# Performance work log

Measured on AMD Instinct MI355X. Metric: run time of the kernel, lower is better.

The kernel has to match this reference:

```python
import jax, jax.numpy as jnp
import numpy as np

D_MODEL = 1024
NUM_HEADS = 16
D_K = D_MODEL // NUM_HEADS
NEG_INF = -1000000000.0  # matches masked_fill value in the torch source


def setup_inputs() -> dict:
    key = jax.random.key(0)
    ks = jax.random.split(key, 12)
    B, S, D = 2, 2048, D_MODEL
    scale = 1.0 / np.sqrt(D)
    inp = {
        "query": jax.random.normal(ks[0], (B, S, D), dtype=jnp.float32),
        "key": jax.random.normal(ks[1], (B, S, D), dtype=jnp.float32),
        "value": jax.random.normal(ks[2], (B, S, D), dtype=jnp.float32),
        # causal mask, broadcast like the torch module: 2D -> [1,1,S,S]
        "mask": jnp.tril(jnp.ones((S, S), dtype=jnp.int32)),
        "wq": jax.random.normal(ks[3], (D, D), dtype=jnp.float32) * scale,
        "bq": jnp.zeros((D,), dtype=jnp.float32),
        "wk": jax.random.normal(ks[4], (D, D), dtype=jnp.float32) * scale,
        "bk": jnp.zeros((D,), dtype=jnp.float32),
        "wv": jax.random.normal(ks[5], (D, D), dtype=jnp.float32) * scale,
        "bv": jnp.zeros((D,), dtype=jnp.float32),
        "wo": jax.random.normal(ks[6], (D, D), dtype=jnp.float32) * scale,
        "bo": jnp.zeros((D,), dtype=jnp.float32),
    }
    return inp


def reference(query, key, value, mask, wq, bq, wk, bk, wv, bv, wo, bo):
    B, S, D = query.shape
    H, dk = NUM_HEADS, D_K

    def proj(x, w, b):
        # nn.Linear: x @ W^T + b, then split heads -> [B, H, S, dk]
        y = jnp.einsum('bsd,ed->bse', x, w) + b
        return y.reshape(B, -1, H, dk).transpose(0, 2, 1, 3)

    Q = proj(query, wq, bq)
    K = proj(key, wk, bk)
    V = proj(value, wv, bv)

    scores = jnp.einsum('bhqd,bhkd->bhqk', Q, K) / jnp.sqrt(jnp.float32(dk))
    m = mask[None, None, :, :]  # 2D mask broadcast as in torch module
    scores = jnp.where(m == 0, jnp.float32(NEG_INF), scores)
    attn_weights = jax.nn.softmax(scores, axis=-1)
    # dropout is identity in eval mode (deterministic reference)
    attn_out = jnp.einsum('bhqk,bhkd->bhqd', attn_weights, V)
    attn_out = attn_out.transpose(0, 2, 1, 3).reshape(B, -1, D)
    output = jnp.einsum('bsd,ed->bse', attn_out, wo) + bo
    return output, attn_weights
```

## Files before the change

### kernel.cpp

```cpp
#include <hip/hip_runtime.h>
#include <stdint.h>

#define S_LEN 2048
#define DM    1024
#define NH    16
#define DK    64
#define MTOT  4096

typedef __bf16 bf16x8 __attribute__((ext_vector_type(8)));
typedef float  f32x4  __attribute__((ext_vector_type(4)));
typedef float  f32x4n __attribute__((ext_vector_type(4)));
typedef unsigned short ushort8v __attribute__((ext_vector_type(8)));
typedef __attribute__((address_space(3))) char lds_char;

static __device__ __forceinline__ unsigned short f2bf(float f){
  uint32_t u = __builtin_bit_cast(uint32_t, f);
  return (unsigned short)((u + 0x7FFFu + ((u >> 16) & 1u)) >> 16);
}

static __device__ __forceinline__ void gl_lds16(const char* g, lds_char* l){
  __builtin_amdgcn_global_load_lds(
      (const __attribute__((address_space(1))) void*)g,
      (__attribute__((address_space(3))) void*)l, 16, 0, 0);
}

#define WAITVM0() asm volatile("s_waitcnt vmcnt(0)" ::: "memory")

template<int ROWB>
static __device__ __forceinline__ void stage_tile(const char* g, int gstride, lds_char* lds, int wid, int lane){
#pragma unroll
  for (int j = 0; j < 4; ++j){
    int c = wid*4 + j;
    int r, cb;
    if (ROWB == 128){ r = c*8 + (lane>>3); cb = (lane&7)*16; }
    else            { r = c*4 + (lane>>4); cb = (lane&15)*16; }
    int cbs = cb ^ ((r&7)<<4);
    gl_lds16(g + (size_t)r*gstride + cbs, lds + c*1024 + lane*16);
  }
}
static __device__ __forceinline__ void stage_k8(const char* g, int gstride, lds_char* lds, int wid, int lane){
#pragma unroll
  for (int j = 0; j < 2; ++j){
    int c = wid*2 + j, r = c*8 + (lane>>3), cb = (lane&7)*16;
    gl_lds16(g + (size_t)r*gstride + (cb ^ ((r&7)<<4)), lds + c*1024 + lane*16);
  }
}
static __device__ __forceinline__ void stage_v8(const char* g, lds_char* lds, int wid, int lane){
#pragma unroll
  for (int j = 0; j < 2; ++j){
    int c = wid*2 + j, r = c*4 + (lane>>4), cb = (lane&15)*16;
    gl_lds16(g + (size_t)r*4096 + (cb ^ ((r&7)<<4)), lds + c*1024 + lane*16);
  }
}

template<int ROWB>
static __device__ __forceinline__ bf16x8 frag_ld(const char* lds, int row, int cb){
  int off = row*ROWB + (cb ^ ((row&7)<<4));
  uint4 v = *reinterpret_cast<const uint4*>(lds + off);
  return __builtin_bit_cast(bf16x8, v);
}

#define MFMA(a,b,c) __builtin_amdgcn_mfma_f32_16x16x32_bf16((a),(b),(c),0,0,0)

__global__ void cvt3(const float* __restrict__ a, const float* __restrict__ b, const float* __restrict__ c,
                     unsigned short* oa, unsigned short* ob, unsigned short* oc, int n8){
  int i = blockIdx.x*256 + threadIdx.x;
  if (i >= n8) return;
  int z = blockIdx.z;
  const float* in = (z==0)?a:((z==1)?b:c);
  unsigned short* out = (z==0)?oa:((z==1)?ob:oc);
  const float4* p = reinterpret_cast<const float4*>(in) + (size_t)i*2;
  float4 x = p[0], y = p[1];
  ushort8v o;
  o[0]=f2bf(x.x); o[1]=f2bf(x.y); o[2]=f2bf(x.z); o[3]=f2bf(x.w);
  o[4]=f2bf(y.x); o[5]=f2bf(y.y); o[6]=f2bf(y.z); o[7]=f2bf(y.w);
  reinterpret_cast<ushort8v*>(out)[i] = o;
}
__global__ void cvt4(const float* __restrict__ a, const float* __restrict__ b,
                     const float* __restrict__ c, const float* __restrict__ d,
                     unsigned short* oa, unsigned short* ob, unsigned short* oc, unsigned short* od, int n8){
  int i = blockIdx.x*256 + threadIdx.x;
  if (i >= n8) return;
  int z = blockIdx.z;
  const float* in = (z==0)?a:((z==1)?b:((z==2)?c:d));
  unsigned short* out = (z==0)?oa:((z==1)?ob:((z==2)?oc:od));
  const float4* p = reinterpret_cast<const float4*>(in) + (size_t)i*2;
  float4 x = p[0], y = p[1];
  ushort8v o;
  o[0]=f2bf(x.x); o[1]=f2bf(x.y); o[2]=f2bf(x.z); o[3]=f2bf(x.w);
  o[4]=f2bf(y.x); o[5]=f2bf(y.y); o[6]=f2bf(y.z); o[7]=f2bf(y.w);
  reinterpret_cast<ushort8v*>(out)[i] = o;
}

static __device__ __forceinline__ void gemm_core(const char* Ag, const char* Wg,
                                                 char* As, char* Bs,
                                                 int wid, int lane, int wr, int wc,
                                                 f32x4 acc[4][4]){
#pragma unroll 1
  for (int kt = 0; kt < 16; ++kt){
    __syncthreads();
    stage_tile<128>(Ag + kt*128, 2048, (lds_char*)As, wid, lane);
    stage_tile<128>(Wg + kt*128, 2048, (lds_char*)Bs, wid, lane);
    WAITVM0();
    __syncthreads();
#pragma unroll
    for (int ks = 0; ks < 2; ++ks){
      int cb = ks*64 + (lane>>4)*16;
      bf16x8 af[4], bfr[4];
#pragma unroll
      for (int mf = 0; mf < 4; ++mf) af[mf]  = frag_ld<128>(As, wr*64 + mf*16 + (lane&15), cb);
#pragma unroll
      for (int nf = 0; nf < 4; ++nf) bfr[nf] = frag_ld<128>(Bs, wc*64 + nf*16 + (lane&15), cb);
      __builtin_amdgcn_s_setprio(1);
#pragma unroll
      for (int mf = 0; mf < 4; ++mf)
#pragma unroll
        for (int nf = 0; nf < 4; ++nf)
          acc[mf][nf] = MFMA(af[mf], bfr[nf], acc[mf][nf]);
      __builtin_amdgcn_s_setprio(0);
    }
  }
}

__global__ void proj_qkv(const unsigned short* Xq, const unsigned short* Xk, const unsigned short* Xv,
                         const unsigned short* Wq, const unsigned short* Wk, const unsigned short* Wv,
                         const float* bq, const float* bk, const float* bv,
                         unsigned short* Qh, unsigned short* Kh, unsigned short* Vt){
  __shared__ __align__(16) char As[16384], Bs[16384];
  int tid = threadIdx.x, wid = tid>>6, lane = tid&63, wr = wid>>1, wc = wid&1;
  int n0 = blockIdx.x*128, m0 = blockIdx.y*128, z = blockIdx.z;
  const unsigned short* X = (z==0)?Xq:((z==1)?Xk:Xv);
  const unsigned short* W = (z==0)?Wq:((z==1)?Wk:Wv);
  const float* bias = (z==0)?bq:((z==1)?bk:bv);
  f32x4 acc[4][4] = {};
  gemm_core((const char*)X + (size_t)m0*2048, (const char*)W + (size_t)n0*2048, As, Bs, wid, lane, wr, wc, acc);
  float bb[4];
#pragma unroll
  for (int nf=0;nf<4;++nf) bb[nf] = bias[n0 + wc*64 + nf*16 + (lane&15)];
  if (z < 2){
    unsigned short* dst = (z==0) ? Qh : Kh;
    float scl = (z==0) ? 0.125f : 1.0f;
#pragma unroll
    for (int mf=0;mf<4;++mf)
#pragma unroll
      for (int nf=0;nf<4;++nf)
#pragma unroll
        for (int i=0;i<4;++i){
          int m = m0 + wr*64 + mf*16 + ((lane>>4)<<2) + i;
          int n = n0 + wc*64 + nf*16 + (lane&15);
          int b = m >> 11, s = m & 2047, h = n >> 6, d = n & 63;
          dst[(((size_t)(b*NH + h)*S_LEN) + s)*DK + d] = f2bf((acc[mf][nf][i] + bb[nf])*scl);
        }
  } else {
#pragma unroll
    for (int mf=0;mf<4;++mf)
#pragma unroll
      for (int nf=0;nf<4;++nf){
        int mb = m0 + wr*64 + mf*16 + ((lane>>4)<<2);
        int n  = n0 + wc*64 + nf*16 + (lane&15);
        int b = mb >> 11, s = mb & 2047, h = n >> 6, d = n & 63;
        ushort4 pk;
        pk.x = f2bf(acc[mf][nf][0] + bb[nf]);
        pk.y = f2bf(acc[mf][nf][1] + bb[nf]);
        pk.z = f2bf(acc[mf][nf][2] + bb[nf]);
        pk.w = f2bf(acc[mf][nf][3] + bb[nf]);
        *reinterpret_cast<ushort4*>(&Vt[(((size_t)(b*NH + h)*DK) + d)*S_LEN + s]) = pk;
      }
  }
}

__global__ void __launch_bounds__(512,1)
flash(const unsigned short* Qh, const unsigned short* Kh, const unsigned short* Vt,
      float* Crow, unsigned short* AO){
  __shared__ __align__(16) char Ks[16384], Vs[16384], Ps[32768];
  __shared__ float sm[2][128], sl[2][128];
  int tid = threadIdx.x, wid = tid>>6, lane = tid&63;
  int rg = wid>>1, wc = wid&1;
  int bh = blockIdx.y, b = bh >> 4, h = bh & 15;
  const char* Kg = (const char*)Kh + (size_t)bh*S_LEN*128;
  const char* Vg = (const char*)Vt + (size_t)bh*DK*4096;
  char* Pw = Ps + wid*4096;

#pragma unroll 1
  for (int half = 0; half < 2; ++half){
    int qt = half ? (int)blockIdx.x : 15 - (int)blockIdx.x;
    stage_k8((const char*)Qh + ((size_t)(bh*S_LEN + qt*128))*128, 128, (lds_char*)Vs, wid, lane);
    WAITVM0();
    __syncthreads();
    bf16x8 qf[2][2];
#pragma unroll
    for (int mf=0;mf<2;++mf)
#pragma unroll
      for (int ks=0;ks<2;++ks)
        qf[mf][ks] = frag_ld<128>(Vs, rg*32 + mf*16 + (lane&15), ks*64 + (lane>>4)*16);
    float mreg[2][4], lreg[2][4];
#pragma unroll
    for (int mf=0;mf<2;++mf)
#pragma unroll
      for (int i=0;i<4;++i){ mreg[mf][i] = -1e30f; lreg[mf][i] = 0.f; }
    f32x4 oacc[2][4] = {};
#pragma unroll 1
    for (int kt = 0; kt <= qt; ++kt){
      __syncthreads();
      stage_k8(Kg + (size_t)kt*16384, 128, (lds_char*)Ks, wid, lane);
      stage_v8(Vg + (size_t)kt*256, (lds_char*)Vs, wid, lane);
      WAITVM0();
      __syncthreads();
      f32x4 sacc[2][4] = {};
#pragma unroll
      for (int ks=0;ks<2;++ks){
        int cb = ks*64 + (lane>>4)*16;
        bf16x8 kf[4];
#pragma unroll
        for (int nf=0;nf<4;++nf) kf[nf] = frag_ld<128>(Ks, wc*64 + nf*16 + (lane&15), cb);
        __builtin_amdgcn_s_setprio(1);
#pragma unroll
        for (int mf=0;mf<2;++mf)
#pragma unroll
          for (int nf=0;nf<4;++nf)
            sacc[mf][nf] = MFMA(qf[mf][ks], kf[nf], sacc[mf][nf]);
        __builtin_amdgcn_s_setprio(0);
      }
      bool diag = (kt == qt);
#pragma unroll
      for (int mf=0;mf<2;++mf)
#pragma unroll
        for (int i=0;i<4;++i){
          int rl = mf*16 + ((lane>>4)<<2) + i;
          int ql = rg*32 + rl;
          float sv[4]; float tmax = -1e30f;
#pragma unroll
          for (int nf=0;nf<4;++nf){
            float x = sacc[mf][nf][i];
            if (diag){ int kl = wc*64 + nf*16 + (lane&15); if (kl > ql) x = -1e30f; }
            sv[nf] = x; tmax = fmaxf(tmax, x);
          }
          tmax = fmaxf(tmax, __shfl_xor(tmax, 1));
          tmax = fmaxf(tmax, __shfl_xor(tmax, 2));
          tmax = fmaxf(tmax, __shfl_xor(tmax, 4));
          tmax = fmaxf(tmax, __shfl_xor(tmax, 8));
          float mo = mreg[mf][i];
          float mn = fmaxf(mo, tmax);
          float e  = __expf(mo - mn);
          float en[4]; float ps = 0.f;
#pragma unroll
          for (int nf=0;nf<4;++nf){
            float ev = __expf(sv[nf]-mn);
            en[nf] = (sv[nf] < -1e29f) ? 0.f : ev;
            ps += en[nf];
          }
          ps += __shfl_xor(ps, 1);
          ps += __shfl_xor(ps, 2);
          ps += __shfl_xor(ps, 4);
          ps += __shfl_xor(ps, 8);
          lreg[mf][i] = lreg[mf][i]*e + ps;
          mreg[mf][i] = mn;
#pragma unroll
          for (int nf=0;nf<4;++nf) oacc[mf][nf][i] *= e;
#pragma unroll
          for (int nf=0;nf<4;++nf){
            int col = nf*16 + (lane&15);
            *reinterpret_cast<unsigned short*>(Pw + rl*128 + ((col*2) ^ ((rl&7)<<4))) = f2bf(en[nf]);
          }
        }
      asm volatile("s_waitcnt lgkmcnt(0)" ::: "memory");
      __builtin_amdgcn_sched_barrier(0);
#pragma unroll
      for (int ks2=0;ks2<2;++ks2){
        bf16x8 pa[2], vb[4];
#pragma unroll
        for (int mf=0;mf<2;++mf) pa[mf] = frag_ld<128>(Pw, mf*16 + (lane&15), ks2*64 + (lane>>4)*16);
#pragma unroll
        for (int nf=0;nf<4;++nf) vb[nf] = frag_ld<256>(Vs, nf*16 + (lane&15), wc*128 + ks2*64 + (lane>>4)*16);
        __builtin_amdgcn_s_setprio(1);
#pragma unroll
        for (int mf=0;mf<2;++mf)
#pragma unroll
          for (int nf=0;nf<4;++nf)
            oacc[mf][nf] = MFMA(pa[mf], vb[nf], oacc[mf][nf]);
        __builtin_amdgcn_s_setprio(0);
      }
    }
    __syncthreads();
    if ((lane & 15) == 0){
#pragma unroll
      for (int mf=0;mf<2;++mf)
#pragma unroll
        for (int i=0;i<4;++i){
          int r = rg*32 + mf*16 + ((lane>>4)<<2) + i;
          sm[wc][r] = mreg[mf][i];
          sl[wc][r] = lreg[mf][i];
        }
    }
    __syncthreads();
    if (tid < 128){
      float m0v = sm[0][tid], m1v = sm[1][tid];
      float mm = fmaxf(m0v, m1v);
      float lF = sl[0][tid]*__expf(m0v - mm) + sl[1][tid]*__expf(m1v - mm);
      Crow[(size_t)bh*S_LEN + qt*128 + tid] = mm + __logf(lF);
    }
    float* Of = reinterpret_cast<float*>(Ps);
#pragma unroll
    for (int mf=0;mf<2;++mf)
#pragma unroll
      for (int i=0;i<4;++i){
        int r = rg*32 + mf*16 + ((lane>>4)<<2) + i;
        float m0v = sm[0][r], m1v = sm[1][r];
        float mm = fmaxf(m0v, m1v);
        float lF = sl[0][r]*__expf(m0v - mm) + sl[1][r]*__expf(m1v - mm);
        float f = __expf(mreg[mf][i] - mm) / lF;
#pragma unroll
        for (int nf=0;nf<4;++nf) oacc[mf][nf][i] *= f;
      }
    if (wc == 1){
#pragma unroll
      for (int mf=0;mf<2;++mf)
#pragma unroll
        for (int nf=0;nf<4;++nf)
#pragma unroll
          for (int i=0;i<4;++i)
            Of[(rg*32 + mf*16 + ((lane>>4)<<2) + i)*64 + nf*16 + (lane&15)] = oacc[mf][nf][i];
    }
    __syncthreads();
    if (wc == 0){
#pragma unroll
      for (int mf=0;mf<2;++mf)
#pragma unroll
        for (int nf=0;nf<4;++nf)
#pragma unroll
          for (int i=0;i<4;++i){
            int r = rg*32 + mf*16 + ((lane>>4)<<2) + i;
            int d = nf*16 + (lane&15);
            float v = oacc[mf][nf][i] + Of[r*64 + d];
            AO[((size_t)(b*S_LEN + qt*128 + r))*DM + h*DK + d] = f2bf(v);
          }
    }
    __syncthreads();
  }
}

__global__ void __launch_bounds__(256,4)
pwrite(const unsigned short* Qh, const unsigned short* Kh, const float* Crow,
       float* __restrict__ attnW){
  int kt = blockIdx.x, qt = blockIdx.y, bh = blockIdx.z;
  int tid = threadIdx.x;
  float* tbase = attnW + ((size_t)(bh*S_LEN + qt*128))*S_LEN + (size_t)kt*128;
  if (kt > qt){
    f32x4n z = (f32x4n)(0.f);
#pragma unroll
    for (int it = 0; it < 16; ++it){
      int idx = it*1024 + tid*4;
      int row = idx >> 7, col = idx & 127;
      *reinterpret_cast<f32x4n*>(tbase + (size_t)row*S_LEN + col) = z;
    }
    return;
  }
  __shared__ __align__(16) char Qs[16384], Ks[16384];
  int wid = tid>>6, lane = tid&63, wr = wid>>1, wc = wid&1;
  stage_tile<128>((const char*)Qh + ((size_t)(bh*S_LEN + qt*128))*128, 128, (lds_char*)Qs, wid, lane);
  stage_tile<128>((const char*)Kh + ((size_t)(bh*S_LEN + kt*128))*128, 128, (lds_char*)Ks, wid, lane);
  WAITVM0();
  __syncthreads();
  f32x4 sacc[4][4] = {};
#pragma unroll
  for (int ks=0;ks<2;++ks){
    int cb = ks*64 + (lane>>4)*16;
    bf16x8 qf[4], kf[4];
#pragma unroll
    for (int mf=0;mf<4;++mf) qf[mf] = frag_ld<128>(Qs, wr*64 + mf*16 + (lane&15), cb);
#pragma unroll
    for (int nf=0;nf<4;++nf) kf[nf] = frag_ld<128>(Ks, wc*64 + nf*16 + (lane&15), cb);
#pragma unroll
    for (int mf=0;mf<4;++mf)
#pragma unroll
      for (int nf=0;nf<4;++nf)
        sacc[mf][nf] = MFMA(qf[mf], kf[nf], sacc[mf][nf]);
  }
  bool diag = (kt == qt);
#pragma unroll
  for (int mf=0;mf<4;++mf)
#pragma unroll
    for (int i=0;i<4;++i){
      int ql = wr*64 + mf*16 + ((lane>>4)<<2) + i;
      float cr = Crow[(size_t)bh*S_LEN + qt*128 + ql];
#pragma unroll
      for (int nf=0;nf<4;++nf){
        int kl = wc*64 + nf*16 + (lane&15);
        float x = sacc[mf][nf][i];
        float p = (diag && kl > ql) ? 0.f : __expf(x - cr);
        tbase[(size_t)ql*S_LEN + kl] = p;
      }
    }
}

__global__ void gemm_out_k(const unsigned short* AOb, const unsigned short* Wo, const float* bo,
                           float* __restrict__ out){
  __shared__ __align__(16) char As[16384], Bs[16384];
  int tid = threadIdx.x, wid = tid>>6, lane = tid&63, wr = wid>>1, wc = wid&1;
  int n0 = blockIdx.x*128, m0 = blockIdx.y*128;
  f32x4 acc[4][4] = {};
  gemm_core((const char*)AOb + (size_t)m0*2048, (const char*)Wo + (size_t)n0*2048, As, Bs, wid, lane, wr, wc, acc);
  float bb[4];
#pragma unroll
  for (int nf=0;nf<4;++nf) bb[nf] = bo[n0 + wc*64 + nf*16 + (lane&15)];
#pragma unroll
  for (int mf=0;mf<4;++mf)
#pragma unroll
    for (int nf=0;nf<4;++nf)
#pragma unroll
      for (int i=0;i<4;++i){
        int m = m0 + wr*64 + mf*16 + ((lane>>4)<<2) + i;
        int n = n0 + wc*64 + nf*16 + (lane&15);
        out[(size_t)m*DM + n] = acc[mf][nf][i] + bb[nf];
      }
}

extern "C" void kernel_launch(void* const* d_in, const int* in_sizes, int n_in,
                              void* d_out, int out_size, void* d_ws, size_t ws_size,
                              hipStream_t stream) {
  (void)in_sizes; (void)n_in; (void)out_size; (void)ws_size;
  const float* query = (const float*)d_in[0];
  const float* key   = (const float*)d_in[1];
  const float* value = (const float*)d_in[2];
  const float* wq = (const float*)d_in[4];
  const float* bq = (const float*)d_in[5];
  const float* wk = (const float*)d_in[6];
  const float* bk = (const float*)d_in[7];
  const float* wv = (const float*)d_in[8];
  const float* bv = (const float*)d_in[9];
  const float* wo = (const float*)d_in[10];
  const float* bo = (const float*)d_in[11];
  float* out   = (float*)d_out;
  float* attnW = out + (size_t)MTOT*DM;

  char* w = (char*)d_ws;
  unsigned short* Xq = (unsigned short*)(w + 0);
  unsigned short* Xk = (unsigned short*)(w + 8388608);
  unsigned short* Xv = (unsigned short*)(w + 16777216);
  unsigned short* Wq = (unsigned short*)(w + 25165824);
  unsigned short* Wk = (unsigned short*)(w + 27262976);
  unsigned short* Wv = (unsigned short*)(w + 29360128);
  unsigned short* Wo = (unsigned short*)(w + 31457280);
  unsigned short* Qh = (unsigned short*)(w + 33554432);
  unsigned short* Kh = (unsigned short*)(w + 41943040);
  unsigned short* Vt = (unsigned short*)(w + 50331648);
  unsigned short* AO = (unsigned short*)(w + 58720256);
  float*          Cr = (float*)         (w + 0);

  { dim3 g(2048,1,3);  cvt3<<<g, dim3(256), 0, stream>>>(query, key, value, Xq, Xk, Xv, 524288); }
  { dim3 g(512,1,4);   cvt4<<<g, dim3(256), 0, stream>>>(wq, wk, wv, wo, Wq, Wk, Wv, Wo, 131072); }
  { dim3 g(8,32,3);    proj_qkv<<<g, dim3(256), 0, stream>>>(Xq, Xk, Xv, Wq, Wk, Wv, bq, bk, bv, Qh, Kh, Vt); }
  { dim3 g(8,32,1);    flash<<<g, dim3(512), 0, stream>>>(Qh, Kh, Vt, Cr, AO); }
  { dim3 g(16,16,32);  pwrite<<<g, dim3(256), 0, stream>>>(Qh, Kh, Cr, attnW); }
  { dim3 g(8,32,1);    gemm_out_k<<<g, dim3(256), 0, stream>>>(AO, Wo, bo, out); }
}
```

Measured before the change: 270.7 us.

## Double-buffer K/V tiles in flash attention and remap grid block ordering

The flash kernel gets two LDS buffers each for K and V, so the next tile's global-to-LDS load is issued before computing on the current tile, overlapping memory with MFMA work and removing one barrier per iteration. Separately, the grid axes of proj_qkv, flash, pwrite and gemm_out_k are swapped so consecutive block IDs walk along M or batch-head first, changing L2/MALL locality and dispatch order across CUs. The double buffering doubles K/V LDS use in flash, which holds one block per CU anyway.

```diff
diff --git a/kernel.cpp b/kernel.cpp
--- a/kernel.cpp
+++ b/kernel.cpp
@@ -128,7 +128,7 @@
                          unsigned short* Qh, unsigned short* Kh, unsigned short* Vt){
   __shared__ __align__(16) char As[16384], Bs[16384];
   int tid = threadIdx.x, wid = tid>>6, lane = tid&63, wr = wid>>1, wc = wid&1;
-  int n0 = blockIdx.x*128, m0 = blockIdx.y*128, z = blockIdx.z;
+  int m0 = blockIdx.x*128, n0 = blockIdx.y*128, z = blockIdx.z;
   const unsigned short* X = (z==0)?Xq:((z==1)?Xk:Xv);
   const unsigned short* W = (z==0)?Wq:((z==1)?Wk:Wv);
   const float* bias = (z==0)?bq:((z==1)?bk:bv);
@@ -172,19 +172,20 @@
 __global__ void __launch_bounds__(512,1)
 flash(const unsigned short* Qh, const unsigned short* Kh, const unsigned short* Vt,
       float* Crow, unsigned short* AO){
-  __shared__ __align__(16) char Ks[16384], Vs[16384], Ps[32768];
+  __shared__ __align__(16) char Ks0[16384], Ks1[16384], Vs0[16384], Vs1[16384], Ps[32768];
   __shared__ float sm[2][128], sl[2][128];
   int tid = threadIdx.x, wid = tid>>6, lane = tid&63;
   int rg = wid>>1, wc = wid&1;
-  int bh = blockIdx.y, b = bh >> 4, h = bh & 15;
+  int bh = blockIdx.x, px = blockIdx.y;
+  int b = bh >> 4, h = bh & 15;
   const char* Kg = (const char*)Kh + (size_t)bh*S_LEN*128;
   const char* Vg = (const char*)Vt + (size_t)bh*DK*4096;
   char* Pw = Ps + wid*4096;
 
 #pragma unroll 1
   for (int half = 0; half < 2; ++half){
-    int qt = half ? (int)blockIdx.x : 15 - (int)blockIdx.x;
-    stage_k8((const char*)Qh + ((size_t)(bh*S_LEN + qt*128))*128, 128, (lds_char*)Vs, wid, lane);
+    int qt = half ? px : 15 - px;
+    stage_k8((const char*)Qh + ((size_t)(bh*S_LEN + qt*128))*128, 128, (lds_char*)Vs1, wid, lane);
     WAITVM0();
     __syncthreads();
     bf16x8 qf[2][2];
@@ -192,27 +193,31 @@
     for (int mf=0;mf<2;++mf)
 #pragma unroll
       for (int ks=0;ks<2;++ks)
-        qf[mf][ks] = frag_ld<128>(Vs, rg*32 + mf*16 + (lane&15), ks*64 + (lane>>4)*16);
+        qf[mf][ks] = frag_ld<128>(Vs1, rg*32 + mf*16 + (lane&15), ks*64 + (lane>>4)*16);
     float mreg[2][4], lreg[2][4];
 #pragma unroll
     for (int mf=0;mf<2;++mf)
 #pragma unroll
       for (int i=0;i<4;++i){ mreg[mf][i] = -1e30f; lreg[mf][i] = 0.f; }
     f32x4 oacc[2][4] = {};
+    char *KsC = Ks0, *KsN = Ks1, *VsC = Vs0, *VsN = Vs1;
+    stage_k8(Kg, 128, (lds_char*)KsC, wid, lane);
+    stage_v8(Vg, (lds_char*)VsC, wid, lane);
 #pragma unroll 1
     for (int kt = 0; kt <= qt; ++kt){
-      __syncthreads();
-      stage_k8(Kg + (size_t)kt*16384, 128, (lds_char*)Ks, wid, lane);
-      stage_v8(Vg + (size_t)kt*256, (lds_char*)Vs, wid, lane);
       WAITVM0();
       __syncthreads();
+      if (kt < qt){
+        stage_k8(Kg + (size_t)(kt+1)*16384, 128, (lds_char*)KsN, wid, lane);
+        stage_v8(Vg + (size_t)(kt+1)*256, (lds_char*)VsN, wid, lane);
+      }
       f32x4 sacc[2][4] = {};
 #pragma unroll
       for (int ks=0;ks<2;++ks){
         int cb = ks*64 + (lane>>4)*16;
         bf16x8 kf[4];
 #pragma unroll
-        for (int nf=0;nf<4;++nf) kf[nf] = frag_ld<128>(Ks, wc*64 + nf*16 + (lane&15), cb);
+        for (int nf=0;nf<4;++nf) kf[nf] = frag_ld<128>(KsC, wc*64 + nf*16 + (lane&15), cb);
         __builtin_amdgcn_s_setprio(1);
 #pragma unroll
         for (int mf=0;mf<2;++mf)
@@ -271,7 +276,7 @@
 #pragma unroll
         for (int mf=0;mf<2;++mf) pa[mf] = frag_ld<128>(Pw, mf*16 + (lane&15), ks2*64 + (lane>>4)*16);
 #pragma unroll
-        for (int nf=0;nf<4;++nf) vb[nf] = frag_ld<256>(Vs, nf*16 + (lane&15), wc*128 + ks2*64 + (lane>>4)*16);
+        for (int nf=0;nf<4;++nf) vb[nf] = frag_ld<256>(VsC, nf*16 + (lane&15), wc*128 + ks2*64 + (lane>>4)*16);
         __builtin_amdgcn_s_setprio(1);
 #pragma unroll
         for (int mf=0;mf<2;++mf)
@@ -280,6 +285,8 @@
             oacc[mf][nf] = MFMA(pa[mf], vb[nf], oacc[mf][nf]);
         __builtin_amdgcn_s_setprio(0);
       }
+      char* t1 = KsC; KsC = KsN; KsN = t1;
+      char* t2 = VsC; VsC = VsN; VsN = t2;
     }
     __syncthreads();
     if ((lane & 15) == 0){
@@ -342,7 +349,7 @@
 __global__ void __launch_bounds__(256,4)
 pwrite(const unsigned short* Qh, const unsigned short* Kh, const float* Crow,
        float* __restrict__ attnW){
-  int kt = blockIdx.x, qt = blockIdx.y, bh = blockIdx.z;
+  int bh = blockIdx.x, qt = blockIdx.y, kt = blockIdx.z;
   int tid = threadIdx.x;
   float* tbase = attnW + ((size_t)(bh*S_LEN + qt*128))*S_LEN + (size_t)kt*128;
   if (kt > qt){
@@ -397,7 +404,7 @@
                            float* __restrict__ out){
   __shared__ __align__(16) char As[16384], Bs[16384];
   int tid = threadIdx.x, wid = tid>>6, lane = tid&63, wr = wid>>1, wc = wid&1;
-  int n0 = blockIdx.x*128, m0 = blockIdx.y*128;
+  int m0 = blockIdx.x*128, n0 = blockIdx.y*128;
   f32x4 acc[4][4] = {};
   gemm_core((const char*)AOb + (size_t)m0*2048, (const char*)Wo + (size_t)n0*2048, As, Bs, wid, lane, wr, wc, acc);
   float bb[4];
@@ -449,8 +456,8 @@
 
   { dim3 g(2048,1,3);  cvt3<<<g, dim3(256), 0, stream>>>(query, key, value, Xq, Xk, Xv, 524288); }
   { dim3 g(512,1,4);   cvt4<<<g, dim3(256), 0, stream>>>(wq, wk, wv, wo, Wq, Wk, Wv, Wo, 131072); }
-  { dim3 g(8,32,3);    proj_qkv<<<g, dim3(256), 0, stream>>>(Xq, Xk, Xv, Wq, Wk, Wv, bq, bk, bv, Qh, Kh, Vt); }
-  { dim3 g(8,32,1);    flash<<<g, dim3(512), 0, stream>>>(Qh, Kh, Vt, Cr, AO); }
-  { dim3 g(16,16,32);  pwrite<<<g, dim3(256), 0, stream>>>(Qh, Kh, Cr, attnW); }
-  { dim3 g(8,32,1);    gemm_out_k<<<g, dim3(256), 0, stream>>>(AO, Wo, bo, out); }
-}
+  { dim3 g(32,8,3);    proj_qkv<<<g, dim3(256), 0, stream>>>(Xq, Xk, Xv, Wq, Wk, Wv, bq, bk, bv, Qh, Kh, Vt); }
+  { dim3 g(32,8,1);    flash<<<g, dim3(512), 0, stream>>>(Qh, Kh, Vt, Cr, AO); }
+  { dim3 g(32,16,16);  pwrite<<<g, dim3(256), 0, stream>>>(Qh, Kh, Cr, attnW); }
+  { dim3 g(32,8,1);    gemm_out_k<<<g, dim3(256), 0, stream>>>(AO, Wo, bo, out); }
+}
```

Result: slower. 283.7 us (+4.8%).
